# Performance work log

Hardware: AMD Instinct MI355X
Metric: run time of the kernel (lower is better)

## Reference

```python
import jax, jax.numpy as jnp
import numpy as np

N = 50000          # nodes
E = 1_600_000      # edges (avg degree 32)
FEAT = 128         # nfeat == nhid
HID = 128
L = 3              # nconvs
C = 10             # nclass
G = 128            # graphs in batch
BN_EPS = 1e-5


def setup_inputs() -> dict:
    key = jax.random.key(0)
    ks = jax.random.split(key, 8)
    x = jax.random.normal(ks[0], (N, FEAT), dtype=jnp.float32)
    edge_index = jax.random.randint(ks[1], (2, E), 0, N, dtype=jnp.int64)
    batch = jnp.sort(jax.random.randint(ks[2], (N,), 0, G, dtype=jnp.int64))
    # stacked per-layer MLP params (nfeat == nhid so shapes are uniform)
    W1 = jax.random.normal(ks[3], (L, FEAT, HID), dtype=jnp.float32) * 0.05
    b1 = jnp.zeros((L, HID), dtype=jnp.float32)
    W2 = jax.random.normal(ks[4], (L, HID, HID), dtype=jnp.float32) * 0.05
    b2 = jnp.zeros((L, HID), dtype=jnp.float32)
    # BatchNorm (eval mode: running stats)
    gamma = jnp.ones((L, HID), dtype=jnp.float32)
    beta = jnp.zeros((L, HID), dtype=jnp.float32)
    rmean = jnp.zeros((L, HID), dtype=jnp.float32)
    rvar = jnp.ones((L, HID), dtype=jnp.float32)
    fc_w = jax.random.normal(ks[5], (HID, C), dtype=jnp.float32) * 0.05
    fc_b = jnp.zeros((C,), dtype=jnp.float32)
    return {
        "x": x, "edge_index": edge_index, "batch": batch,
        "W1": W1, "b1": b1, "W2": W2, "b2": b2,
        "gamma": gamma, "beta": beta, "rmean": rmean, "rvar": rvar,
        "fc_w": fc_w, "fc_b": fc_b,
    }


def reference(x, edge_index, batch, W1, b1, W2, b2, gamma, beta, rmean, rvar, fc_w, fc_b):
    src, dst = edge_index[0], edge_index[1]
    for l in range(L):
        # GINConv aggregation: h_i = (1 + eps) * x_i + sum_{j -> i} x_j  (eps = 0)
        agg = jax.ops.segment_sum(x[src], dst, num_segments=N)  # [N, d] scatter-add
        h = x + agg
        # MLP: Linear -> ReLU -> Linear -> BatchNorm (eval: running stats)
        h = jax.nn.relu(h @ W1[l] + b1[l])
        h = h @ W2[l] + b2[l]
        h = (h - rmean[l]) * jax.lax.rsqrt(rvar[l] + BN_EPS) * gamma[l] + beta[l]
        # outer ReLU; dropout is identity at inference
        x = jax.nn.relu(h)
    # global mean pool over batch ids
    counts = jax.ops.segment_sum(jnp.ones((N,), x.dtype), batch, num_segments=G)
    pooled = jax.ops.segment_sum(x, batch, num_segments=G)
    pooled = pooled / jnp.clip(counts, 1.0)[:, None]  # [G, HID]
    logits = pooled @ fc_w + fc_b                      # [G, C]
    return jax.nn.log_softmax(logits, axis=1)
```

## Files before the change

kernel.cpp:

```cpp
#include <hip/hip_runtime.h>

#define NN 50000
#define EE 1600000
#define GG 128
#define NC 10

#define SB_N   49
#define SB_PAD 36864
#define BK_N   782
#define BK_PAD 2560
#define CHUNK  4096
#define NBLK1  391
#define SLICES 9

typedef __attribute__((ext_vector_type(8))) short bf16x8;
typedef __attribute__((ext_vector_type(4))) float f32x4;
typedef unsigned short u16;

__device__ inline u16 f2bf(float x){
  unsigned u = __builtin_bit_cast(unsigned, x);
  u += 0x7fffu + ((u >> 16) & 1u);
  return (u16)(u >> 16);
}
__device__ inline float bf2f(u16 u){
  return __builtin_bit_cast(float, ((unsigned)u) << 16);
}

__global__ void k_zero_int(int* __restrict__ p, int n){
  int i = blockIdx.x * 256 + threadIdx.x;
  if (i < n) p[i] = 0;
}

__global__ __launch_bounds__(256) void k_scatL1(const int* __restrict__ srcI, const int* __restrict__ dstI,
                                                int* __restrict__ scur, int* __restrict__ sstg){
  __shared__ int hist[SB_N];
  __shared__ int base[64];
  __shared__ int gadj[SB_N];
  __shared__ unsigned reo[CHUNK];
  int t = threadIdx.x;
  int e0 = blockIdx.x * CHUNK;
  int cnt = EE - e0; if (cnt > CHUNK) cnt = CHUNK;
  if (t < SB_N) hist[t] = 0;
  __syncthreads();
  unsigned p[16]; int rk[16];
  #pragma unroll
  for (int r = 0; r < 16; ++r){
    int i = r * 256 + t;
    if (i < cnt){
      unsigned d = (unsigned)dstI[e0 + i];
      p[r] = (d << 16) | (unsigned)srcI[e0 + i];
      rk[r] = atomicAdd(&hist[d >> 10], 1);
    }
  }
  __syncthreads();
  if (t < 64) base[t] = (t < SB_N) ? hist[t] : 0;
  __syncthreads();
  for (int off = 1; off < 64; off <<= 1){
    int a = (t < 64 && t >= off) ? base[t - off] : 0;
    __syncthreads();
    if (t < 64) base[t] += a;
    __syncthreads();
  }
  if (t < SB_N){
    int ex = base[t] - hist[t];
    gadj[t] = atomicAdd(&scur[t], hist[t]) - ex;
  }
  __syncthreads();
  #pragma unroll
  for (int r = 0; r < 16; ++r){
    int i = r * 256 + t;
    if (i < cnt){
      unsigned sb = p[r] >> 26;
      reo[(base[sb] - hist[sb]) + rk[r]] = p[r];
    }
  }
  __syncthreads();
  for (int q = t; q < cnt; q += 256){
    unsigned v = reo[q];
    unsigned sb = v >> 26;
    int off = gadj[sb] + q;
    if ((unsigned)off < SB_PAD) sstg[sb * SB_PAD + off] = (int)v;
  }
}

__global__ __launch_bounds__(256) void k_scatL2(const int* __restrict__ sstg, const int* __restrict__ scur,
                                                int* __restrict__ bcur, int* __restrict__ bstg){
  __shared__ int hist[16];
  __shared__ int base[16];
  __shared__ int gadj[16];
  __shared__ unsigned reo[CHUNK];
  int t = threadIdx.x;
  int sb = blockIdx.x / SLICES;
  int sl = blockIdx.x % SLICES;
  int ssz = scur[sb]; if (ssz > SB_PAD) ssz = SB_PAD;
  int i0 = sl * CHUNK;
  int cnt = ssz - i0;
  if (cnt <= 0) return;
  if (cnt > CHUNK) cnt = CHUNK;
  if (t < 16) hist[t] = 0;
  __syncthreads();
  unsigned p[16]; int rk[16];
  #pragma unroll
  for (int r = 0; r < 16; ++r){
    int i = r * 256 + t;
    if (i < cnt){
      p[r] = (unsigned)sstg[sb * SB_PAD + i0 + i];
      rk[r] = atomicAdd(&hist[(p[r] >> 22) & 15], 1);
    }
  }
  __syncthreads();
  if (t < 16) base[t] = hist[t];
  __syncthreads();
  for (int off = 1; off < 16; off <<= 1){
    int a = (t < 16 && t >= off) ? base[t - off] : 0;
    __syncthreads();
    if (t < 16) base[t] += a;
    __syncthreads();
  }
  if (t < 16){
    int ex = base[t] - hist[t];
    gadj[t] = atomicAdd(&bcur[sb * 16 + t], hist[t]) - ex;
  }
  __syncthreads();
  #pragma unroll
  for (int r = 0; r < 16; ++r){
    int i = r * 256 + t;
    if (i < cnt){
      unsigned b = (p[r] >> 22) & 15;
      reo[(base[b] - hist[b]) + rk[r]] = p[r];
    }
  }
  __syncthreads();
  for (int q = t; q < cnt; q += 256){
    unsigned v = reo[q];
    unsigned b = (v >> 22) & 15;
    int off = gadj[b] + q;
    if ((unsigned)off < BK_PAD) bstg[(sb * 16 + b) * BK_PAD + off] = (int)v;
  }
}

__global__ __launch_bounds__(256) void k_finalize(const int* __restrict__ bstg, const int* __restrict__ bcur,
                                                  u16* __restrict__ adj, int2* __restrict__ ndinfo){
  __shared__ unsigned ebuf[BK_PAD];
  __shared__ int hist[64];
  __shared__ int lrs[64];
  __shared__ int lcur[64];
  int b = blockIdx.x;
  int t = threadIdx.x;
  int bsz = bcur[b]; if (bsz > BK_PAD) bsz = BK_PAD;
  if (t < 64) hist[t] = 0;
  __syncthreads();
  for (int i = t; i < bsz; i += 256){
    unsigned p = (unsigned)bstg[b * BK_PAD + i];
    ebuf[i] = p;
    atomicAdd(&hist[(p >> 16) & 63], 1);
  }
  __syncthreads();
  if (t < 64) lrs[t] = hist[t];
  __syncthreads();
  for (int off = 1; off < 64; off <<= 1){
    int a = (t < 64 && t >= off) ? lrs[t - off] : 0;
    __syncthreads();
    if (t < 64) lrs[t] += a;
    __syncthreads();
  }
  if (t < 64){
    int ex = lrs[t] - hist[t];
    lcur[t] = ex;
    int node = b * 64 + t;
    if (node < NN) ndinfo[node] = make_int2(b * BK_PAD + ex, hist[t]);
  }
  __syncthreads();
  for (int i = t; i < bsz; i += 256){
    unsigned p = ebuf[i];
    int slot = atomicAdd(&lcur[(p >> 16) & 63], 1);
    adj[b * BK_PAD + slot] = (u16)(p & 0xffffu);
  }
}

__global__ void k_cvt_x(const float* __restrict__ x, u16* __restrict__ xb){
  int i = blockIdx.x * 256 + threadIdx.x;
  float4 v = ((const float4*)x)[i];
  ushort4 o;
  o.x = f2bf(v.x); o.y = f2bf(v.y); o.z = f2bf(v.z); o.w = f2bf(v.w);
  ((ushort4*)xb)[i] = o;
}

__global__ void k_prep_w(const float* __restrict__ W1, const float* __restrict__ W2,
                         u16* __restrict__ Wt){
  int i = blockIdx.x * 256 + threadIdx.x;
  int a = i >> 14; int r = i & 16383; int n = r >> 7; int k = r & 127;
  const float* Wsrc = (a < 3) ? (W1 + a * 16384) : (W2 + (a - 3) * 16384);
  Wt[a * 16384 + n * 128 + k] = f2bf(Wsrc[k * 128 + n]);
}

__global__ void k_prep_scsh(const float* __restrict__ b1, const float* __restrict__ b2,
                            const float* __restrict__ gma, const float* __restrict__ bta,
                            const float* __restrict__ rmn, const float* __restrict__ rvr,
                            float* __restrict__ SC, float* __restrict__ SH){
  int i = blockIdx.x * 256 + threadIdx.x;
  if (i < 768){
    int l = i >> 8; int r = i & 255; int mode = r >> 7; int c = r & 127;
    if (mode == 0){
      SC[(l * 2) * 128 + c] = 1.0f;
      SH[(l * 2) * 128 + c] = b1[l * 128 + c];
    } else {
      float S = gma[l * 128 + c] * rsqrtf(rvr[l * 128 + c] + 1e-5f);
      SC[(l * 2 + 1) * 128 + c] = S;
      SH[(l * 2 + 1) * 128 + c] = (b2[l * 128 + c] - rmn[l * 128 + c]) * S + bta[l * 128 + c];
    }
  }
}

__global__ __launch_bounds__(256) void k_agg(const u16* __restrict__ xb, u16* __restrict__ hb,
                                             const u16* __restrict__ adj,
                                             const int2* __restrict__ ndinfo){
  int t = threadIdx.x;
  int node = blockIdx.x * 8 + (t >> 5);
  int lane = t & 31;
  const ushort4* xv = (const ushort4*)xb;
  ushort4 sv = xv[(long)node * 32 + lane];
  float a0 = bf2f(sv.x), a1 = bf2f(sv.y), a2 = bf2f(sv.z), a3 = bf2f(sv.w);
  int2 nd = ndinfo[node];
  int r0 = nd.x;
  int d  = nd.y;
  int j = 0;
  for (; j + 4 <= d; j += 4){
    int s0 = adj[r0 + j + 0];
    int s1 = adj[r0 + j + 1];
    int s2 = adj[r0 + j + 2];
    int s3 = adj[r0 + j + 3];
    ushort4 v0 = xv[(long)s0 * 32 + lane];
    ushort4 v1 = xv[(long)s1 * 32 + lane];
    ushort4 v2 = xv[(long)s2 * 32 + lane];
    ushort4 v3 = xv[(long)s3 * 32 + lane];
    a0 += bf2f(v0.x) + bf2f(v1.x) + bf2f(v2.x) + bf2f(v3.x);
    a1 += bf2f(v0.y) + bf2f(v1.y) + bf2f(v2.y) + bf2f(v3.y);
    a2 += bf2f(v0.z) + bf2f(v1.z) + bf2f(v2.z) + bf2f(v3.z);
    a3 += bf2f(v0.w) + bf2f(v1.w) + bf2f(v2.w) + bf2f(v3.w);
  }
  for (; j < d; ++j){
    int s0 = adj[r0 + j];
    ushort4 v0 = xv[(long)s0 * 32 + lane];
    a0 += bf2f(v0.x); a1 += bf2f(v0.y); a2 += bf2f(v0.z); a3 += bf2f(v0.w);
  }
  ushort4 o;
  o.x = f2bf(a0); o.y = f2bf(a1); o.z = f2bf(a2); o.w = f2bf(a3);
  ((ushort4*)hb)[(long)node * 32 + lane] = o;
}

__global__ __launch_bounds__(256, 2) void k_gemm(const u16* __restrict__ Ain,
                                                 const u16* __restrict__ Wt,
                                                 const float* __restrict__ SC,
                                                 const float* __restrict__ SH,
                                                 u16* __restrict__ Out){
  int gw = (blockIdx.x * 256 + threadIdx.x) >> 6;
  int l  = threadIdx.x & 63;
  int m  = l & 15;
  int kb = l >> 4;
  const int NW = (gridDim.x * 256) >> 6;

  bf16x8 w[8][4];
  #pragma unroll
  for (int mt = 0; mt < 8; ++mt)
    #pragma unroll
    for (int ks = 0; ks < 4; ++ks)
      w[mt][ks] = *(const bf16x8*)(Wt + (mt * 16 + m) * 128 + ks * 32 + kb * 8);

  for (int tile = gw; tile < 3125; tile += NW){
    long row0 = (long)tile * 16;
    f32x4 acc[8] = {};
    #pragma unroll
    for (int ks = 0; ks < 4; ++ks){
      bf16x8 h = *(const bf16x8*)(Ain + (row0 + m) * 128 + ks * 32 + kb * 8);
      #pragma unroll
      for (int mt = 0; mt < 8; ++mt)
        acc[mt] = __builtin_amdgcn_mfma_f32_16x16x32_bf16(w[mt][ks], h, acc[mt], 0, 0, 0);
    }
    #pragma unroll
    for (int mt = 0; mt < 8; ++mt){
      int c0 = mt * 16 + kb * 4;
      float4 sc = *(const float4*)(SC + c0);
      float4 sh = *(const float4*)(SH + c0);
      float v0 = fmaxf(acc[mt][0] * sc.x + sh.x, 0.f);
      float v1 = fmaxf(acc[mt][1] * sc.y + sh.y, 0.f);
      float v2 = fmaxf(acc[mt][2] * sc.z + sh.z, 0.f);
      float v3 = fmaxf(acc[mt][3] * sc.w + sh.w, 0.f);
      ushort4 o;
      o.x = f2bf(v0); o.y = f2bf(v1); o.z = f2bf(v2); o.w = f2bf(v3);
      *(ushort4*)(Out + (row0 + m) * 128 + c0) = o;
    }
  }
}

__global__ __launch_bounds__(256) void k_pool(const u16* __restrict__ xb,
                                              const int* __restrict__ batch,
                                              float* __restrict__ pooled){
  int g = blockIdx.x;
  int lo, hi;
  { int a = 0, b = NN; while (a < b){ int mm = (a + b) >> 1; if (batch[mm] < g) a = mm + 1; else b = mm; } lo = a; }
  { int a = lo, b = NN; while (a < b){ int mm = (a + b) >> 1; if (batch[mm] < g + 1) a = mm + 1; else b = mm; } hi = a; }
  int t = threadIdx.x;
  int c = t & 127;
  int half = t >> 7;
  float acc = 0.f;
  for (int i = lo + half; i < hi; i += 2) acc += bf2f(xb[(long)i * 128 + c]);
  __shared__ float s[256];
  s[t] = acc;
  __syncthreads();
  if (t < 128){
    float v = s[t] + s[t + 128];
    int cnt = hi - lo;
    float denom = (cnt > 0) ? (float)cnt : 1.0f;
    pooled[g * 128 + t] = v / denom;
  }
}

__global__ void k_head(const float* __restrict__ pooled, const float* __restrict__ fcw,
                       const float* __restrict__ fcb, float* __restrict__ out){
  int g = threadIdx.x;
  float logit[NC];
  #pragma unroll
  for (int c = 0; c < NC; ++c) logit[c] = fcb[c];
  for (int k = 0; k < 128; ++k){
    float pv = pooled[g * 128 + k];
    #pragma unroll
    for (int c = 0; c < NC; ++c) logit[c] += pv * fcw[k * NC + c];
  }
  float m = logit[0];
  #pragma unroll
  for (int c = 1; c < NC; ++c) m = fmaxf(m, logit[c]);
  float sum = 0.f;
  #pragma unroll
  for (int c = 0; c < NC; ++c) sum += expf(logit[c] - m);
  float ls = logf(sum);
  #pragma unroll
  for (int c = 0; c < NC; ++c) out[g * NC + c] = logit[c] - m - ls;
}

extern "C" void kernel_launch(void* const* d_in, const int* in_sizes, int n_in,
                              void* d_out, int out_size, void* d_ws, size_t ws_size,
                              hipStream_t stream) {
  const float* x     = (const float*)d_in[0];
  const int*   eidx  = (const int*)  d_in[1];
  const int*   batch = (const int*)  d_in[2];
  const float* W1    = (const float*)d_in[3];
  const float* b1    = (const float*)d_in[4];
  const float* W2    = (const float*)d_in[5];
  const float* b2    = (const float*)d_in[6];
  const float* gma   = (const float*)d_in[7];
  const float* bta   = (const float*)d_in[8];
  const float* rmn   = (const float*)d_in[9];
  const float* rvr   = (const float*)d_in[10];
  const float* fcw   = (const float*)d_in[11];
  const float* fcb   = (const float*)d_in[12];
  float* out = (float*)d_out;

  const int* srcI = eidx;
  const int* dstI = eidx + EE;

  u16* bufX = (u16*)d_ws;
  u16* bufA = bufX + 6400000;
  u16* bufB = bufA + 6400000;
  u16* Wt   = bufB + 6400000;
  float* SC = (float*)(Wt + 98304);
  float* SH = SC + 768;
  float* pooled = SH + 768;
  u16* adj  = (u16*)(pooled + 16384);
  int2* ndinfo = (int2*)(adj + (BK_N * BK_PAD));
  int* ctr  = (int*)(ndinfo + 50048);
  int* scur = ctr;
  int* bcur = ctr + 64;
  int* sstg = (int*)bufA;
  int* bstg = (int*)bufB;

  k_zero_int<<<4, 256, 0, stream>>>(ctr, 64 + 784);
  k_scatL1  <<<NBLK1, 256, 0, stream>>>(srcI, dstI, scur, sstg);
  k_scatL2  <<<SB_N * SLICES, 256, 0, stream>>>(sstg, scur, bcur, bstg);
  k_finalize<<<BK_N, 256, 0, stream>>>(bstg, bcur, adj, ndinfo);

  k_cvt_x    <<<6250, 256, 0, stream>>>(x, bufX);
  k_prep_w   <<<384, 256, 0, stream>>>(W1, W2, Wt);
  k_prep_scsh<<<3, 256, 0, stream>>>(b1, b2, gma, bta, rmn, rvr, SC, SH);

  u16* aggin [3] = { bufX, bufA, bufB };
  u16* aggout[3] = { bufA, bufB, bufA };
  u16* g0out [3] = { bufB, bufX, bufX };
  u16* g1out [3] = { bufA, bufB, bufA };

  for (int l = 0; l < 3; ++l){
    k_agg <<<6250, 256, 0, stream>>>(aggin[l], aggout[l], adj, ndinfo);
    k_gemm<<<256, 256, 0, stream>>>(aggout[l], Wt + l * 16384,
                                    SC + (l * 2) * 128, SH + (l * 2) * 128, g0out[l]);
    k_gemm<<<256, 256, 0, stream>>>(g0out[l], Wt + (3 + l) * 16384,
                                    SC + (l * 2 + 1) * 128, SH + (l * 2 + 1) * 128, g1out[l]);
  }

  k_pool<<<GG, 256, 0, stream>>>(g1out[2], batch, pooled);
  k_head<<<1, 128, 0, stream>>>(pooled, fcw, fcb, out);
}
```

Before: 440.4 us.

## Widen aggregation loads to 16B and parallelize mean-pool over node chunks

The aggregation kernel now has 16 lanes per node, each loading 8 bf16 values (16 bytes), so every block covers 16 nodes and the grid is halved. The mean-pool is restructured: each of 782 blocks sums a 64-node chunk, keeps per-graph partials in registers for up to three graphs, reduces them through shared memory, and atomically adds into a pooled buffer that is now zeroed up front. The per-graph count lookup and the division by it move into the head kernel. The aim is fewer, wider gather loads and much more parallel pooling than the old one-block-per-graph serial loop, at the cost of float atomics and nondeterministic summation order.

```diff
diff --git a/kernel.cpp b/kernel.cpp
--- a/kernel.cpp
+++ b/kernel.cpp
@@ -216,11 +216,13 @@
                                              const u16* __restrict__ adj,
                                              const int2* __restrict__ ndinfo){
   int t = threadIdx.x;
-  int node = blockIdx.x * 8 + (t >> 5);
-  int lane = t & 31;
-  const ushort4* xv = (const ushort4*)xb;
-  ushort4 sv = xv[(long)node * 32 + lane];
-  float a0 = bf2f(sv.x), a1 = bf2f(sv.y), a2 = bf2f(sv.z), a3 = bf2f(sv.w);
+  int node = blockIdx.x * 16 + (t >> 4);
+  int lane = t & 15;
+  const bf16x8* xv = (const bf16x8*)xb;
+  bf16x8 sv = xv[(long)node * 16 + lane];
+  float a[8];
+  #pragma unroll
+  for (int j = 0; j < 8; ++j) a[j] = bf2f((u16)sv[j]);
   int2 nd = ndinfo[node];
   int r0 = nd.x;
   int d  = nd.y;
@@ -230,23 +232,24 @@
     int s1 = adj[r0 + j + 1];
     int s2 = adj[r0 + j + 2];
     int s3 = adj[r0 + j + 3];
-    ushort4 v0 = xv[(long)s0 * 32 + lane];
-    ushort4 v1 = xv[(long)s1 * 32 + lane];
-    ushort4 v2 = xv[(long)s2 * 32 + lane];
-    ushort4 v3 = xv[(long)s3 * 32 + lane];
-    a0 += bf2f(v0.x) + bf2f(v1.x) + bf2f(v2.x) + bf2f(v3.x);
-    a1 += bf2f(v0.y) + bf2f(v1.y) + bf2f(v2.y) + bf2f(v3.y);
-    a2 += bf2f(v0.z) + bf2f(v1.z) + bf2f(v2.z) + bf2f(v3.z);
-    a3 += bf2f(v0.w) + bf2f(v1.w) + bf2f(v2.w) + bf2f(v3.w);
+    bf16x8 v0 = xv[(long)s0 * 16 + lane];
+    bf16x8 v1 = xv[(long)s1 * 16 + lane];
+    bf16x8 v2 = xv[(long)s2 * 16 + lane];
+    bf16x8 v3 = xv[(long)s3 * 16 + lane];
+    #pragma unroll
+    for (int q = 0; q < 8; ++q)
+      a[q] += bf2f((u16)v0[q]) + bf2f((u16)v1[q]) + bf2f((u16)v2[q]) + bf2f((u16)v3[q]);
   }
   for (; j < d; ++j){
     int s0 = adj[r0 + j];
-    ushort4 v0 = xv[(long)s0 * 32 + lane];
-    a0 += bf2f(v0.x); a1 += bf2f(v0.y); a2 += bf2f(v0.z); a3 += bf2f(v0.w);
-  }
-  ushort4 o;
-  o.x = f2bf(a0); o.y = f2bf(a1); o.z = f2bf(a2); o.w = f2bf(a3);
-  ((ushort4*)hb)[(long)node * 32 + lane] = o;
+    bf16x8 v0 = xv[(long)s0 * 16 + lane];
+    #pragma unroll
+    for (int q = 0; q < 8; ++q) a[q] += bf2f((u16)v0[q]);
+  }
+  bf16x8 o;
+  #pragma unroll
+  for (int j2 = 0; j2 < 8; ++j2) o[j2] = (short)f2bf(a[j2]);
+  ((bf16x8*)hb)[(long)node * 16 + lane] = o;
 }
 
 __global__ __launch_bounds__(256, 2) void k_gemm(const u16* __restrict__ Ain,
@@ -296,34 +299,66 @@
 __global__ __launch_bounds__(256) void k_pool(const u16* __restrict__ xb,
                                               const int* __restrict__ batch,
                                               float* __restrict__ pooled){
-  int g = blockIdx.x;
+  __shared__ float4 red[8][32];
+  int b = blockIdx.x;
+  int n0 = b << 6;
+  int t = threadIdx.x;
+  int lane = t & 31;
+  int rg = t >> 5;
+  int g0 = batch[n0];
+  int lastn = n0 + 63; if (lastn >= NN) lastn = NN - 1;
+  int nk = batch[lastn] - g0;
+  const ushort4* xv = (const ushort4*)xb;
+  float4 a0 = {0,0,0,0}, a1 = {0,0,0,0}, a2 = {0,0,0,0};
+  int rbase = n0 + rg * 8;
+  #pragma unroll
+  for (int i = 0; i < 8; ++i){
+    int r = rbase + i;
+    if (r >= NN) break;
+    int k = batch[r] - g0;
+    ushort4 v = xv[(long)r * 32 + lane];
+    float fx = bf2f(v.x), fy = bf2f(v.y), fz = bf2f(v.z), fw = bf2f(v.w);
+    if (k == 0){ a0.x += fx; a0.y += fy; a0.z += fz; a0.w += fw; }
+    else if (k == 1){ a1.x += fx; a1.y += fy; a1.z += fz; a1.w += fw; }
+    else if (k == 2){ a2.x += fx; a2.y += fy; a2.z += fz; a2.w += fw; }
+    else {
+      float* pg = pooled + (g0 + k) * 128 + lane * 4;
+      atomicAdd(pg + 0, fx); atomicAdd(pg + 1, fy);
+      atomicAdd(pg + 2, fz); atomicAdd(pg + 3, fw);
+    }
+  }
+  int kmax = (nk < 2) ? nk : 2;
+  for (int k = 0; k <= kmax; ++k){
+    red[rg][lane] = (k == 0) ? a0 : ((k == 1) ? a1 : a2);
+    __syncthreads();
+    if (t < 32){
+      float4 s = red[0][t];
+      #pragma unroll
+      for (int r = 1; r < 8; ++r){
+        float4 q = red[r][t];
+        s.x += q.x; s.y += q.y; s.z += q.z; s.w += q.w;
+      }
+      float* pg = pooled + (g0 + k) * 128 + t * 4;
+      atomicAdd(pg + 0, s.x); atomicAdd(pg + 1, s.y);
+      atomicAdd(pg + 2, s.z); atomicAdd(pg + 3, s.w);
+    }
+    __syncthreads();
+  }
+}
+
+__global__ void k_head(const float* __restrict__ pooled, const float* __restrict__ fcw,
+                       const float* __restrict__ fcb, const int* __restrict__ batch,
+                       float* __restrict__ out){
+  int g = threadIdx.x;
   int lo, hi;
   { int a = 0, b = NN; while (a < b){ int mm = (a + b) >> 1; if (batch[mm] < g) a = mm + 1; else b = mm; } lo = a; }
   { int a = lo, b = NN; while (a < b){ int mm = (a + b) >> 1; if (batch[mm] < g + 1) a = mm + 1; else b = mm; } hi = a; }
-  int t = threadIdx.x;
-  int c = t & 127;
-  int half = t >> 7;
-  float acc = 0.f;
-  for (int i = lo + half; i < hi; i += 2) acc += bf2f(xb[(long)i * 128 + c]);
-  __shared__ float s[256];
-  s[t] = acc;
-  __syncthreads();
-  if (t < 128){
-    float v = s[t] + s[t + 128];
-    int cnt = hi - lo;
-    float denom = (cnt > 0) ? (float)cnt : 1.0f;
-    pooled[g * 128 + t] = v / denom;
-  }
-}
-
-__global__ void k_head(const float* __restrict__ pooled, const float* __restrict__ fcw,
-                       const float* __restrict__ fcb, float* __restrict__ out){
-  int g = threadIdx.x;
+  float inv = 1.0f / fmaxf((float)(hi - lo), 1.0f);
   float logit[NC];
   #pragma unroll
   for (int c = 0; c < NC; ++c) logit[c] = fcb[c];
   for (int k = 0; k < 128; ++k){
-    float pv = pooled[g * 128 + k];
+    float pv = pooled[g * 128 + k] * inv;
     #pragma unroll
     for (int c = 0; c < NC; ++c) logit[c] += pv * fcw[k * NC + c];
   }
@@ -366,15 +401,16 @@
   float* SC = (float*)(Wt + 98304);
   float* SH = SC + 768;
   float* pooled = SH + 768;
-  u16* adj  = (u16*)(pooled + 16384);
-  int2* ndinfo = (int2*)(adj + (BK_N * BK_PAD));
-  int* ctr  = (int*)(ndinfo + 50048);
+  int* ctr  = (int*)(pooled + 16384);
   int* scur = ctr;
   int* bcur = ctr + 64;
+  u16* adj  = (u16*)(ctr + 848);
+  int2* ndinfo = (int2*)(adj + (BK_N * BK_PAD));
   int* sstg = (int*)bufA;
   int* bstg = (int*)bufB;
 
-  k_zero_int<<<4, 256, 0, stream>>>(ctr, 64 + 784);
+  k_zero_int<<<68, 256, 0, stream>>>((int*)pooled, 16384 + 848);
+
   k_scatL1  <<<NBLK1, 256, 0, stream>>>(srcI, dstI, scur, sstg);
   k_scatL2  <<<SB_N * SLICES, 256, 0, stream>>>(sstg, scur, bcur, bstg);
   k_finalize<<<BK_N, 256, 0, stream>>>(bstg, bcur, adj, ndinfo);
@@ -389,13 +425,13 @@
   u16* g1out [3] = { bufA, bufB, bufA };
 
   for (int l = 0; l < 3; ++l){
-    k_agg <<<6250, 256, 0, stream>>>(aggin[l], aggout[l], adj, ndinfo);
+    k_agg <<<3125, 256, 0, stream>>>(aggin[l], aggout[l], adj, ndinfo);
     k_gemm<<<256, 256, 0, stream>>>(aggout[l], Wt + l * 16384,
                                     SC + (l * 2) * 128, SH + (l * 2) * 128, g0out[l]);
     k_gemm<<<256, 256, 0, stream>>>(g0out[l], Wt + (3 + l) * 16384,
                                     SC + (l * 2 + 1) * 128, SH + (l * 2 + 1) * 128, g1out[l]);
   }
 
-  k_pool<<<GG, 256, 0, stream>>>(g1out[2], batch, pooled);
-  k_head<<<1, 128, 0, stream>>>(pooled, fcw, fcb, out);
-}
+  k_pool<<<BK_N, 256, 0, stream>>>(g1out[2], batch, pooled);
+  k_head<<<1, 128, 0, stream>>>(pooled, fcw, fcb, batch, out);
+}
```

Result: faster. 416.5 us (-5.4%).
